# Kernel tuning notes

Hardware: AMD Instinct MI355X
Metric: run time of the kernel (lower is better)

Reference implementation:

```python
import jax, jax.numpy as jnp
import numpy as np

EPS = 1e-8
SMOOTH = 9.0
N_IMAGE, N_REGIONS, N_CAP, MAX_WORDS = 64, 36, 64, 40
EMBED, SIM_DIM = 1024, 256


def l2norm(x, axis=-1):
    n = jnp.sqrt(jnp.sum(x * x, axis=axis, keepdims=True)) + EPS
    return x / n


def setup_inputs() -> dict:
    key = jax.random.key(0)
    k1, k2, k3, k4 = jax.random.split(key, 4)
    img_emb = jax.random.normal(k1, (N_IMAGE, N_REGIONS, EMBED), dtype=jnp.float32)
    cap_emb = jax.random.normal(k2, (N_CAP, MAX_WORDS, EMBED), dtype=jnp.float32)
    cap_lens = jax.random.randint(k3, (N_CAP,), 10, MAX_WORDS + 1)
    # zero out padded words so the batched formulation matches the per-caption loop
    mask = (jnp.arange(MAX_WORDS)[None, :] < cap_lens[:, None]).astype(jnp.float32)
    cap_emb = cap_emb * mask[:, :, None]
    adjs = jnp.zeros((N_CAP, MAX_WORDS, MAX_WORDS), dtype=jnp.int32)
    depends = jnp.zeros((N_CAP, MAX_WORDS, MAX_WORDS), dtype=jnp.int32)
    r = np.sqrt(6.0) / np.sqrt(EMBED + SIM_DIM)
    W = jax.random.uniform(k4, (EMBED, SIM_DIM), minval=-r, maxval=r, dtype=jnp.float32)
    b = jnp.zeros((SIM_DIM,), dtype=jnp.float32)
    return {"img_emb": img_emb, "cap_emb": cap_emb, "cap_lens": cap_lens,
            "adjs": adjs, "depends": depends, "W": W, "b": b}


def reference(img_emb, cap_emb, cap_lens, adjs, depends, W, b):
    C, L, D = cap_emb.shape
    mask = (jnp.arange(L)[None, :] < cap_lens[:, None]).astype(cap_emb.dtype)  # (C, L)
    cap = cap_emb * mask[:, :, None]
    # attn: (C, I, R, L) = context . query^T for every (caption, image) pair
    attn = jnp.einsum('ird,cld->cirl', img_emb, cap)
    attn = jax.nn.leaky_relu(attn, negative_slope=0.1)
    # l2norm over the word dim (padded words contribute exactly 0)
    attn = attn / (jnp.sqrt(jnp.sum(attn * attn, axis=3, keepdims=True)) + EPS)
    # softmax over regions after transpose + smooth scaling: (C, I, L, R)
    attn = jax.nn.softmax(jnp.swapaxes(attn, 2, 3) * SMOOTH, axis=3)
    wc = jnp.einsum('cilr,ird->cild', attn, img_emb)  # (C, I, L, D)
    wc = l2norm(wc, axis=-1)
    sim = jnp.square(wc - cap[:, None, :, :])
    out = l2norm(jax.nn.relu(sim @ W + b), axis=-1)
    # zero padded-word rows (the original returns only :n_word slices)
    out = out * mask[:, None, :, None]
    return out  # (C, I, L, SIM_DIM)
```

## Files before the change

kernel.cpp:

```cpp
#include <hip/hip_runtime.h>

#define C_N 64
#define I_N 64
#define R_N 36
#define L_N 40
#define D_N 1024
#define S_N 256

#define P_LD 72

#define OFF_CAP 2359296
#define OFF_WT  4980736
#define OFF_IMT 5242880
#define OFF_SLK 8388608
#define OFF_SIM 8388672
#define M_ALL   (C_N * I_N * L_N)
#define CH_STRIDE ((size_t)M_ALL * 32)

typedef float f4 __attribute__((ext_vector_type(4)));
typedef short s16x8 __attribute__((ext_vector_type(8)));
typedef short s16x4 __attribute__((ext_vector_type(4)));

__device__ __forceinline__ unsigned short f2bs(float f) {
    union { float f; unsigned u; } v; v.f = f;
    unsigned r = v.u + 0x7FFFu + ((v.u >> 16) & 1u);
    return (unsigned short)(r >> 16);
}
__device__ __forceinline__ float bs2f(unsigned short s) {
    union { unsigned u; float f; } v; v.u = ((unsigned)s) << 16;
    return v.f;
}
__device__ __forceinline__ void async16(const unsigned short* g, unsigned short* l) {
    __builtin_amdgcn_global_load_lds(
        (const __attribute__((address_space(1))) unsigned int*)g,
        (__attribute__((address_space(3))) unsigned int*)l, 16, 0, 0);
}

__global__ void k_convert(const float* __restrict__ img, const float* __restrict__ cap,
                          const float* __restrict__ W, unsigned short* __restrict__ ws) {
    int t = blockIdx.x * 256 + threadIdx.x;
    if (t < I_N * R_N * D_N) ws[t] = f2bs(img[t]);
    if (t < C_N * L_N * D_N) ws[OFF_CAP + t] = f2bs(cap[t]);
    if (t < D_N * S_N) {
        int d = t >> 8, s = t & 255;
        ws[OFF_WT + (((d >> 5) * 256 + s) * 32) + (d & 31)] = f2bs(W[t]);
    }
    if (t < 64) ws[OFF_SLK + t] = 0;
}

__global__ __launch_bounds__(256)
void k_imt(const float* __restrict__ img, unsigned short* __restrict__ imt) {
    __shared__ unsigned short t[64][50];
    const int i = blockIdx.y, d0 = blockIdx.x * 64;
    const int tid = threadIdx.x;
    #pragma unroll
    for (int it = 0; it < 9; ++it) {
        int e = it * 256 + tid;
        int r = e >> 6, dc = e & 63;
        t[dc][r] = f2bs(img[((size_t)i * R_N + r) * D_N + d0 + dc]);
    }
    #pragma unroll
    for (int it = 0; it < 3; ++it) {
        int e = it * 256 + tid;
        t[e & 63][36 + (e >> 6)] = 0;
    }
    __syncthreads();
    #pragma unroll
    for (int it = 0; it < 6; ++it) {
        int e = it * 256 + tid;
        int dc = e / 24, wd = e - dc * 24;
        unsigned v = (unsigned)t[dc][2 * wd] | ((unsigned)t[dc][2 * wd + 1] << 16);
        ((unsigned*)imt)[(size_t)(i * D_N + d0 + dc) * 24 + wd] = v;
    }
}

__global__ __launch_bounds__(512, 4)
void k_pre(const unsigned short* __restrict__ img_b,
           const unsigned short* __restrict__ cap_b,
           const unsigned short* __restrict__ img_t,
           unsigned short* __restrict__ simg) {
    __shared__ __align__(16) unsigned short s_p[8][48 * P_LD];

    const int n = blockIdx.y * 8 + blockIdx.x;
    const int x = n & 7, m = n >> 3;
    const int i   = ((x & 3) << 4) | (m >> 2);
    const int oct = ((x >> 2) << 2) | (m & 3);
    const int wave = threadIdx.x >> 6, lane = threadIdx.x & 63;
    const int c = oct * 8 + wave;
    const int pair = c * I_N + i;
    const int q = lane >> 4, ln16 = lane & 15;

    const unsigned short* ai = img_b + i * (R_N * D_N);
    const unsigned short* bc = cap_b + c * (L_N * D_N);
    const unsigned short* imtc = img_t + (size_t)i * D_N * 48;
    unsigned short* sp = &s_p[wave][0];

    for (int k = lane; k < 48 * P_LD / 2; k += 64) ((unsigned*)sp)[k] = 0;

    f4 acc[3][3] = {};
    #pragma unroll 4
    for (int ks = 0; ks < 32; ++ks) {
        const int kb = ks * 32 + q * 8;
        s16x8 af[3], bf[3];
        af[0] = *(const s16x8*)(ai + ln16 * D_N + kb);
        af[1] = *(const s16x8*)(ai + (16 + ln16) * D_N + kb);
        af[2] = (ln16 < 4) ? *(const s16x8*)(ai + (32 + ln16) * D_N + kb) : (s16x8)0;
        bf[0] = *(const s16x8*)(bc + ln16 * D_N + kb);
        bf[1] = *(const s16x8*)(bc + (16 + ln16) * D_N + kb);
        bf[2] = (ln16 < 8) ? *(const s16x8*)(bc + (32 + ln16) * D_N + kb) : (s16x8)0;
        #pragma unroll
        for (int mt = 0; mt < 3; ++mt)
            #pragma unroll
            for (int nt = 0; nt < 3; ++nt)
                acc[mt][nt] = __builtin_amdgcn_mfma_f32_16x16x32_bf16(af[mt], bf[nt], acc[mt][nt], 0, 0, 0);
    }

    #pragma unroll
    for (int mt = 0; mt < 3; ++mt)
        #pragma unroll
        for (int nt = 0; nt < 3; ++nt)
            #pragma unroll
            for (int j = 0; j < 4; ++j) {
                float v = acc[mt][nt][j];
                acc[mt][nt][j] = (v > 0.f) ? v : 0.1f * v;
            }
    #pragma unroll
    for (int mt = 0; mt < 3; ++mt)
        #pragma unroll
        for (int j = 0; j < 4; ++j) {
            float ss = 0.f;
            #pragma unroll
            for (int nt = 0; nt < 3; ++nt) ss += acc[mt][nt][j] * acc[mt][nt][j];
            #pragma unroll
            for (int o = 1; o < 16; o <<= 1) ss += __shfl_xor(ss, o, 64);
            float inv = 1.f / (sqrtf(ss) + 1e-8f);
            #pragma unroll
            for (int nt = 0; nt < 3; ++nt) acc[mt][nt][j] *= inv;
        }
    #pragma unroll
    for (int nt = 0; nt < 3; ++nt) {
        const int l = nt * 16 + ln16;
        float mx = -1e30f;
        #pragma unroll
        for (int mt = 0; mt < 3; ++mt)
            #pragma unroll
            for (int j = 0; j < 4; ++j) {
                int r = mt * 16 + q * 4 + j;
                if (r < R_N) mx = fmaxf(mx, 9.f * acc[mt][nt][j]);
            }
        mx = fmaxf(mx, __shfl_xor(mx, 16, 64));
        mx = fmaxf(mx, __shfl_xor(mx, 32, 64));
        float sum = 0.f;
        #pragma unroll
        for (int mt = 0; mt < 3; ++mt)
            #pragma unroll
            for (int j = 0; j < 4; ++j) {
                int r = mt * 16 + q * 4 + j;
                float e = (r < R_N) ? __expf(9.f * acc[mt][nt][j] - mx) : 0.f;
                acc[mt][nt][j] = e;
                sum += e;
            }
        sum += __shfl_xor(sum, 16, 64);
        sum += __shfl_xor(sum, 32, 64);
        float inv = 1.f / sum;
        #pragma unroll
        for (int mt = 0; mt < 3; ++mt)
            #pragma unroll
            for (int j = 0; j < 4; ++j) {
                int r = mt * 16 + q * 4 + j;
                if (r < R_N && l < L_N) sp[l * P_LD + r] = f2bs(acc[mt][nt][j] * inv);
            }
    }

    s16x8 paf[3][2];
    #pragma unroll
    for (int nl = 0; nl < 3; ++nl)
        #pragma unroll
        for (int ks = 0; ks < 2; ++ks)
            paf[nl][ks] = *(const s16x8*)(sp + (nl * 16 + ln16) * P_LD + ks * 32 + q * 8);

    float rs[3] = {};
    #pragma unroll 2
    for (int ch = 0; ch < 32; ++ch) {
        f4 a2[2][3] = {};
        #pragma unroll
        for (int ks = 0; ks < 2; ++ks) {
            const int kb = ks * 32 + q * 8;
            #pragma unroll
            for (int md = 0; md < 2; ++md) {
                const int drow = ch * 32 + md * 16 + ln16;
                s16x8 afr = *(const s16x8*)(imtc + drow * 48 + kb);
                #pragma unroll
                for (int nl = 0; nl < 3; ++nl)
                    a2[md][nl] = __builtin_amdgcn_mfma_f32_16x16x32_bf16(afr, paf[nl][ks], a2[md][nl], 0, 0, 0);
            }
        }
        #pragma unroll
        for (int md = 0; md < 2; ++md)
            #pragma unroll
            for (int nl = 0; nl < 3; ++nl)
                #pragma unroll
                for (int j = 0; j < 4; ++j)
                    rs[nl] += a2[md][nl][j] * a2[md][nl][j];
    }
    float inv2[3];
    #pragma unroll
    for (int nl = 0; nl < 3; ++nl) {
        float s = rs[nl];
        s += __shfl_xor(s, 16, 64);
        s += __shfl_xor(s, 32, 64);
        inv2[nl] = 1.f / (sqrtf(s) + 1e-8f);
    }

    #pragma unroll 2
    for (int ch = 0; ch < 32; ++ch) {
        f4 a2[2][3] = {};
        #pragma unroll
        for (int ks = 0; ks < 2; ++ks) {
            const int kb = ks * 32 + q * 8;
            #pragma unroll
            for (int md = 0; md < 2; ++md) {
                const int drow = ch * 32 + md * 16 + ln16;
                s16x8 afr = *(const s16x8*)(imtc + drow * 48 + kb);
                #pragma unroll
                for (int nl = 0; nl < 3; ++nl)
                    a2[md][nl] = __builtin_amdgcn_mfma_f32_16x16x32_bf16(afr, paf[nl][ks], a2[md][nl], 0, 0, 0);
            }
        }
        const size_t chbase = (size_t)ch * CH_STRIDE + (size_t)pair * L_N * 32;
        #pragma unroll
        for (int nl = 0; nl < 3; ++nl) {
            const int l = nl * 16 + ln16;
            if (l < L_N) {
                const float iv = inv2[nl];
                #pragma unroll
                for (int md = 0; md < 2; ++md) {
                    const int dd = md * 16 + q * 4;
                    const int db = ch * 32 + dd;
                    const s16x4 cv = *(const s16x4*)(bc + l * D_N + db);
                    s16x4 ov;
                    #pragma unroll
                    for (int j = 0; j < 4; ++j) {
                        float dv = a2[md][nl][j] * iv - bs2f((unsigned short)cv[j]);
                        ov[j] = (short)f2bs(dv * dv);
                    }
                    __builtin_nontemporal_store(ov,
                        (s16x4*)(simg + chbase + (size_t)l * 32 + dd));
                }
            }
        }
    }
}

__global__ __launch_bounds__(512, 4)
void k_gemm3(const unsigned short* __restrict__ simt,
             const unsigned short* __restrict__ wtt,
             const int* __restrict__ cap_lens,
             const float* __restrict__ bias,
             float* __restrict__ out) {
    __shared__ __align__(16) unsigned short sA[2][128 * 32];
    __shared__ __align__(16) unsigned short sB[2][256 * 32];
    __shared__ float s_sum[128];

    const int tid = threadIdx.x;
    const int w = tid >> 6, lane = tid & 63;
    const int ln16 = lane & 15, q = lane >> 4;
    const int wm = (w >> 2) * 64, wn = (w & 3) * 64;
    const int m0 = blockIdx.x * 128;
    const int srow = tid >> 2;
    const int swz = ((tid & 3) ^ ((srow >> 1) & 3)) << 3;
    const unsigned short* gA  = simt + ((size_t)(m0 + srow)) * 32 + swz;
    const unsigned short* gB0 = wtt + (size_t)srow * 32 + swz;
    const unsigned short* gB1 = wtt + (size_t)(128 + srow) * 32 + swz;
    unsigned short* const lA = (unsigned short*)sA + tid * 8;
    unsigned short* const lB = (unsigned short*)sB + tid * 8;

    if (tid < 128) s_sum[tid] = 0.f;

    async16(gA, lA);
    async16(gB0, lB);
    async16(gB1, lB + 4096);

    f4 acc[4][4] = {};
    #pragma unroll 1
    for (int kc = 0; kc < 31; ++kc) {
        const int nb = (kc + 1) & 1;
        async16(gA + (size_t)(kc + 1) * CH_STRIDE, lA + nb * 4096);
        async16(gB0 + (kc + 1) * 8192, lB + nb * 8192);
        async16(gB1 + (kc + 1) * 8192, lB + nb * 8192 + 4096);
        asm volatile("s_waitcnt vmcnt(3)" ::: "memory");
        __builtin_amdgcn_s_barrier();
        __builtin_amdgcn_sched_barrier(0);
        const unsigned short* cA = (const unsigned short*)sA + (kc & 1) * 4096;
        const unsigned short* cB = (const unsigned short*)sB + (kc & 1) * 8192;
        s16x8 af[4], bf[4];
        #pragma unroll
        for (int mt = 0; mt < 4; ++mt) {
            int row = wm + mt * 16 + ln16;
            af[mt] = *(const s16x8*)(cA + row * 32 + ((q ^ ((row >> 1) & 3)) << 3));
        }
        #pragma unroll
        for (int nt = 0; nt < 4; ++nt) {
            int row = wn + nt * 16 + ln16;
            bf[nt] = *(const s16x8*)(cB + row * 32 + ((q ^ ((row >> 1) & 3)) << 3));
        }
        #pragma unroll
        for (int mt = 0; mt < 4; ++mt)
            #pragma unroll
            for (int nt = 0; nt < 4; ++nt)
                acc[mt][nt] = __builtin_amdgcn_mfma_f32_16x16x32_bf16(af[mt], bf[nt], acc[mt][nt], 0, 0, 0);
        __builtin_amdgcn_s_barrier();
    }
    asm volatile("s_waitcnt vmcnt(0)" ::: "memory");
    __builtin_amdgcn_s_barrier();
    __builtin_amdgcn_sched_barrier(0);
    {
        const unsigned short* cA = (const unsigned short*)sA + 4096;
        const unsigned short* cB = (const unsigned short*)sB + 8192;
        s16x8 af[4], bf[4];
        #pragma unroll
        for (int mt = 0; mt < 4; ++mt) {
            int row = wm + mt * 16 + ln16;
            af[mt] = *(const s16x8*)(cA + row * 32 + ((q ^ ((row >> 1) & 3)) << 3));
        }
        #pragma unroll
        for (int nt = 0; nt < 4; ++nt) {
            int row = wn + nt * 16 + ln16;
            bf[nt] = *(const s16x8*)(cB + row * 32 + ((q ^ ((row >> 1) & 3)) << 3));
        }
        #pragma unroll
        for (int mt = 0; mt < 4; ++mt)
            #pragma unroll
            for (int nt = 0; nt < 4; ++nt)
                acc[mt][nt] = __builtin_amdgcn_mfma_f32_16x16x32_bf16(af[mt], bf[nt], acc[mt][nt], 0, 0, 0);
    }

    float bv[4];
    #pragma unroll
    for (int nt = 0; nt < 4; ++nt) bv[nt] = bias[wn + nt * 16 + ln16];
    #pragma unroll
    for (int mt = 0; mt < 4; ++mt)
        #pragma unroll
        for (int j = 0; j < 4; ++j) {
            float s = 0.f;
            #pragma unroll
            for (int nt = 0; nt < 4; ++nt) {
                float v = acc[mt][nt][j] + bv[nt];
                v = fmaxf(v, 0.f);
                acc[mt][nt][j] = v;
                s += v * v;
            }
            #pragma unroll
            for (int o = 1; o < 16; o <<= 1) s += __shfl_xor(s, o, 64);
            if (ln16 == 0) atomicAdd(&s_sum[wm + mt * 16 + q * 4 + j], s);
        }
    __syncthreads();
    if (tid < 128) {
        int grow = m0 + tid;
        int c = grow / (I_N * L_N);
        int l = grow % L_N;
        float inv = 1.f / (sqrtf(s_sum[tid]) + 1e-8f);
        s_sum[tid] = (l < cap_lens[c]) ? inv : 0.f;
    }
    __syncthreads();
    #pragma unroll
    for (int mt = 0; mt < 4; ++mt)
        #pragma unroll
        for (int j = 0; j < 4; ++j) {
            const int rt = wm + mt * 16 + q * 4 + j;
            const float sc = s_sum[rt];
            #pragma unroll
            for (int nt = 0; nt < 4; ++nt)
                __builtin_nontemporal_store(acc[mt][nt][j] * sc,
                    &out[(size_t)(m0 + rt) * S_N + wn + nt * 16 + ln16]);
        }
}

extern "C" void kernel_launch(void* const* d_in, const int* in_sizes, int n_in,
                              void* d_out, int out_size, void* d_ws, size_t ws_size,
                              hipStream_t stream) {
    const float* img  = (const float*)d_in[0];
    const float* cap  = (const float*)d_in[1];
    const int*   lens = (const int*)d_in[2];
    const float* W    = (const float*)d_in[5];
    const float* bias = (const float*)d_in[6];
    float* out = (float*)d_out;
    unsigned short* ws = (unsigned short*)d_ws;

    k_convert<<<10240, 256, 0, stream>>>(img, cap, W, ws);
    dim3 gridT(16, I_N);
    k_imt<<<gridT, 256, 0, stream>>>(img, ws + OFF_IMT);

    dim3 gridP(8, I_N);
    k_pre<<<gridP, 512, 0, stream>>>(ws, ws + OFF_CAP, ws + OFF_IMT, ws + OFF_SIM);

    k_gemm3<<<M_ALL / 128, 512, 0, stream>>>(ws + OFF_SIM, ws + OFF_WT, lens, bias, out);
}
```

Measured before the change: 526.1 us.

## Compute weighted-context norms via per-image Gram matrix instead of full GEMM pass

Adds a small kernel that computes the 36x36 Gram matrix of image regions (img·imgᵀ) per image in bf16. The k_pre kernel then gets the squared norm of each weighted-context row as pᵀGp, using a tiny MFMA product with the Gram matrix. This replaces the first full 1024-dimension pass that rebuilt the weighted context only to take its norm. It removes half of the big MFMA work and image-transpose reads, at the cost of an extra launch, extra workspace, and bf16 rounding of the Gram matrix, which may shift the norm slightly.

```diff
diff --git a/kernel.cpp b/kernel.cpp
--- a/kernel.cpp
+++ b/kernel.cpp
@@ -16,6 +16,7 @@
 #define OFF_SIM 8388672
 #define M_ALL   (C_N * I_N * L_N)
 #define CH_STRIDE ((size_t)M_ALL * 32)
+#define OFF_G   (OFF_SIM + 32 * CH_STRIDE)
 
 typedef float f4 __attribute__((ext_vector_type(4)));
 typedef short s16x8 __attribute__((ext_vector_type(8)));
@@ -74,10 +75,45 @@
     }
 }
 
+__global__ __launch_bounds__(64)
+void k_gram(const unsigned short* __restrict__ img_b, unsigned short* __restrict__ g) {
+    const int i = blockIdx.x;
+    const int lane = threadIdx.x;
+    const int q = lane >> 4, ln16 = lane & 15;
+    const unsigned short* ai = img_b + i * (R_N * D_N);
+    unsigned short* gi = g + i * (48 * 64);
+    for (int e = lane; e < 48 * 8; e += 64) {
+        int r = e >> 3, wd = e & 7;
+        ((unsigned*)(gi + r * 64 + 48))[wd] = 0;
+    }
+    f4 c[3][3] = {};
+    #pragma unroll 4
+    for (int ks = 0; ks < 32; ++ks) {
+        const int kb = ks * 32 + q * 8;
+        s16x8 af[3];
+        af[0] = *(const s16x8*)(ai + ln16 * D_N + kb);
+        af[1] = *(const s16x8*)(ai + (16 + ln16) * D_N + kb);
+        af[2] = (ln16 < 4) ? *(const s16x8*)(ai + (32 + ln16) * D_N + kb) : (s16x8)0;
+        #pragma unroll
+        for (int mt = 0; mt < 3; ++mt)
+            #pragma unroll
+            for (int nt = 0; nt < 3; ++nt)
+                c[mt][nt] = __builtin_amdgcn_mfma_f32_16x16x32_bf16(af[mt], af[nt], c[mt][nt], 0, 0, 0);
+    }
+    #pragma unroll
+    for (int mt = 0; mt < 3; ++mt)
+        #pragma unroll
+        for (int nt = 0; nt < 3; ++nt)
+            #pragma unroll
+            for (int j = 0; j < 4; ++j)
+                gi[(mt * 16 + q * 4 + j) * 64 + nt * 16 + ln16] = f2bs(c[mt][nt][j]);
+}
+
 __global__ __launch_bounds__(512, 4)
 void k_pre(const unsigned short* __restrict__ img_b,
            const unsigned short* __restrict__ cap_b,
            const unsigned short* __restrict__ img_t,
+           const unsigned short* __restrict__ gram,
            unsigned short* __restrict__ simg) {
     __shared__ __align__(16) unsigned short s_p[8][48 * P_LD];
 
@@ -179,37 +215,36 @@
         for (int ks = 0; ks < 2; ++ks)
             paf[nl][ks] = *(const s16x8*)(sp + (nl * 16 + ln16) * P_LD + ks * 32 + q * 8);
 
-    float rs[3] = {};
-    #pragma unroll 2
-    for (int ch = 0; ch < 32; ++ch) {
-        f4 a2[2][3] = {};
-        #pragma unroll
-        for (int ks = 0; ks < 2; ++ks) {
-            const int kb = ks * 32 + q * 8;
-            #pragma unroll
-            for (int md = 0; md < 2; ++md) {
-                const int drow = ch * 32 + md * 16 + ln16;
-                s16x8 afr = *(const s16x8*)(imtc + drow * 48 + kb);
-                #pragma unroll
-                for (int nl = 0; nl < 3; ++nl)
-                    a2[md][nl] = __builtin_amdgcn_mfma_f32_16x16x32_bf16(afr, paf[nl][ks], a2[md][nl], 0, 0, 0);
-            }
-        }
-        #pragma unroll
-        for (int md = 0; md < 2; ++md)
+    const unsigned short* gi = gram + i * (48 * 64);
+    f4 T[3][3] = {};
+    #pragma unroll
+    for (int ks = 0; ks < 2; ++ks) {
+        const int kb = ks * 32 + q * 8;
+        s16x8 ga[3];
+        #pragma unroll
+        for (int mt = 0; mt < 3; ++mt)
+            ga[mt] = *(const s16x8*)(gi + (mt * 16 + ln16) * 64 + kb);
+        #pragma unroll
+        for (int mt = 0; mt < 3; ++mt)
             #pragma unroll
             for (int nl = 0; nl < 3; ++nl)
-                #pragma unroll
-                for (int j = 0; j < 4; ++j)
-                    rs[nl] += a2[md][nl][j] * a2[md][nl][j];
+                T[mt][nl] = __builtin_amdgcn_mfma_f32_16x16x32_bf16(ga[mt], paf[nl][ks], T[mt][nl], 0, 0, 0);
     }
     float inv2[3];
     #pragma unroll
     for (int nl = 0; nl < 3; ++nl) {
-        float s = rs[nl];
-        s += __shfl_xor(s, 16, 64);
-        s += __shfl_xor(s, 32, 64);
-        inv2[nl] = 1.f / (sqrtf(s) + 1e-8f);
+        const int l = nl * 16 + ln16;
+        float rsl = 0.f;
+        #pragma unroll
+        for (int mt = 0; mt < 3; ++mt) {
+            const s16x4 pv = *(const s16x4*)(sp + l * P_LD + mt * 16 + q * 4);
+            #pragma unroll
+            for (int j = 0; j < 4; ++j)
+                rsl += bs2f((unsigned short)pv[j]) * T[mt][nl][j];
+        }
+        rsl += __shfl_xor(rsl, 16, 64);
+        rsl += __shfl_xor(rsl, 32, 64);
+        inv2[nl] = 1.f / (sqrtf(rsl) + 1e-8f);
     }
 
     #pragma unroll 2
@@ -390,9 +425,11 @@
     k_convert<<<10240, 256, 0, stream>>>(img, cap, W, ws);
     dim3 gridT(16, I_N);
     k_imt<<<gridT, 256, 0, stream>>>(img, ws + OFF_IMT);
+    k_gram<<<I_N, 64, 0, stream>>>(ws, ws + OFF_G);
 
     dim3 gridP(8, I_N);
-    k_pre<<<gridP, 512, 0, stream>>>(ws, ws + OFF_CAP, ws + OFF_IMT, ws + OFF_SIM);
+    k_pre<<<gridP, 512, 0, stream>>>(ws, ws + OFF_CAP, ws + OFF_IMT, ws + OFF_G,
+                                     ws + OFF_SIM);
 
     k_gemm3<<<M_ALL / 128, 512, 0, stream>>>(ws + OFF_SIM, ws + OFF_WT, lens, bias, out);
 }
```

Result: no change. 521.5 us (-0.9%).
